# Kernel optimization log

Measured on AMD Instinct MI355X. Metric: run time of the kernel, lower is better.

## Reference

```python
import jax, jax.numpy as jnp
import numpy as np

B, DIM, HEADS, AGENT = 16, 256, 8, 49
POOL = 7  # int(sqrt(agent_num))


def _pool_matrix(size, out):
    # PyTorch AdaptiveAvgPool2d bin boundaries: start=floor(i*size/out), end=ceil((i+1)*size/out)
    P = np.zeros((out, size), np.float32)
    for i in range(out):
        s = (i * size) // out
        e = -((-(i + 1) * size) // out)
        P[i, s:e] = 1.0 / (e - s)
    return jnp.asarray(P)


def _forward(x, Wq, Wkv, Wproj, bproj, Wdwc, bdwc,
             an_bias, na_bias, ah_bias, aw_bias, ha_bias, wa_bias, H, W):
    b, c, h, w = x.shape
    n = H * W
    head_dim = c // HEADS
    scale = head_dim ** -0.5
    xt = x.reshape(b, c, n).transpose(0, 2, 1)            # [b, n, c]
    q = xt @ Wq.T                                          # [b, n, c]
    kv = xt @ Wkv.T
    k, v = jnp.split(kv, 2, axis=-1)
    # agent tokens: adaptive avg pool of q over the HxW grid -> 7x7
    qimg = q.reshape(b, H, W, c)
    Ph, Pw = _pool_matrix(H, POOL), _pool_matrix(W, POOL)
    agent = jnp.einsum('ph,qw,bhwc->bpqc', Ph, Pw, qimg).reshape(b, AGENT, c)

    def to_heads(t):
        return t.reshape(b, -1, HEADS, head_dim).transpose(0, 2, 1, 3)

    qh, kh, vh, ah = to_heads(q), to_heads(k), to_heads(v), to_heads(agent)

    # stage 1: agent -> kv attention with interpolated position bias
    pb1 = jax.image.resize(an_bias, (HEADS, AGENT, H, W), method='bilinear').reshape(HEADS, AGENT, n)
    pb2 = (ah_bias + aw_bias).reshape(1, HEADS, AGENT, n)
    pos_bias = pb1[None] + pb2                             # [1/b, h, 49, n]
    agent_attn = jax.nn.softmax(jnp.einsum('bhad,bhnd->bhan', ah * scale, kh) + pos_bias, axis=-1)
    agent_v = jnp.einsum('bhan,bhnd->bhad', agent_attn, vh)  # [b, h, 49, d]

    # stage 2: query -> agent attention
    ab1 = jax.image.resize(na_bias, (HEADS, AGENT, H, W), method='bilinear').reshape(HEADS, AGENT, n).transpose(0, 2, 1)
    ab2 = (ha_bias + wa_bias).reshape(1, HEADS, n, AGENT)
    agent_bias = ab1[None] + ab2                           # [1/b, h, n, 49]
    q_attn = jax.nn.softmax(jnp.einsum('bhnd,bhad->bhna', qh * scale, ah) + agent_bias, axis=-1)
    out = jnp.einsum('bhna,bhad->bhnd', q_attn, agent_v).transpose(0, 2, 1, 3).reshape(b, n, c)

    # depthwise conv residual on v
    vimg = vh.transpose(0, 2, 1, 3).reshape(b, H, W, c).transpose(0, 3, 1, 2)  # [b, c, H, W]
    dw = jax.lax.conv_general_dilated(vimg, Wdwc, (1, 1), 'SAME',
                                      feature_group_count=c,
                                      dimension_numbers=('NCHW', 'OIHW', 'NCHW'))
    dw = dw + bdwc[None, :, None, None]
    out = out + dw.transpose(0, 2, 3, 1).reshape(b, n, c)
    out = out @ Wproj.T + bproj
    return out.transpose(0, 2, 1).reshape(b, c, h, w)


def setup_inputs() -> dict:
    key = jax.random.key(0)
    ks = jax.random.split(key, 12)
    s = 0.02
    return {
        'x': jax.random.normal(ks[0], (B, DIM, 64, 64), jnp.float32),
        'Wq': jax.random.normal(ks[1], (DIM, DIM), jnp.float32) * s,
        'Wkv': jax.random.normal(ks[2], (2 * DIM, DIM), jnp.float32) * s,
        'Wproj': jax.random.normal(ks[3], (DIM, DIM), jnp.float32) * s,
        'bproj': jnp.zeros((DIM,), jnp.float32),
        'Wdwc': jax.random.normal(ks[4], (DIM, 1, 3, 3), jnp.float32) * s,
        'bdwc': jnp.zeros((DIM,), jnp.float32),
        'an_bias': jax.random.normal(ks[5], (HEADS, AGENT, 7, 7), jnp.float32) * s,
        'na_bias': jax.random.normal(ks[6], (HEADS, AGENT, 7, 7), jnp.float32) * s,
        'ah_bias': jax.random.normal(ks[7], (1, HEADS, AGENT, 64, 1), jnp.float32) * s,
        'aw_bias': jax.random.normal(ks[8], (1, HEADS, AGENT, 1, 64), jnp.float32) * s,
        'ha_bias': jax.random.normal(ks[9], (1, HEADS, 64, 1, AGENT), jnp.float32) * s,
        'wa_bias': jax.random.normal(ks[10], (1, HEADS, 1, 64, AGENT), jnp.float32) * s,
        'H': 64,
        'W': 64,
    }


def reference(x, Wq, Wkv, Wproj, bproj, Wdwc, bdwc,
              an_bias, na_bias, ah_bias, aw_bias, ha_bias, wa_bias, H, W):
    return _forward(x, Wq, Wkv, Wproj, bproj, Wdwc, bdwc,
                    an_bias, na_bias, ah_bias, aw_bias, ha_bias, wa_bias, H, W)
```

## Files before the change

### kernel.cpp

```cpp
#include <hip/hip_runtime.h>
#include <hip/hip_bf16.h>
#include <stdint.h>

using bf16 = __hip_bfloat16;

#define SCALE 0.17677669529663687f

typedef short short8 __attribute__((ext_vector_type(8)));
typedef float f32x4 __attribute__((ext_vector_type(4)));

__device__ __forceinline__ float bf2f(bf16 v) { return __bfloat162float(v); }

__device__ __forceinline__ unsigned short f2bf(float f) {
    unsigned int u = __float_as_uint(f);
    unsigned int r = u + 0x7fffu + ((u >> 16) & 1u);
    return (unsigned short)(r >> 16);
}

__device__ __forceinline__ void load8bf(const bf16* p, float* f) {
    uint4 u = *reinterpret_cast<const uint4*>(p);
    f[0] = __uint_as_float(u.x << 16); f[1] = __uint_as_float(u.x & 0xffff0000u);
    f[2] = __uint_as_float(u.y << 16); f[3] = __uint_as_float(u.y & 0xffff0000u);
    f[4] = __uint_as_float(u.z << 16); f[5] = __uint_as_float(u.z & 0xffff0000u);
    f[6] = __uint_as_float(u.w << 16); f[7] = __uint_as_float(u.w & 0xffff0000u);
}

__device__ __forceinline__ void gload16(const void* g, void* l) {
    __builtin_amdgcn_global_load_lds(
        (const __attribute__((address_space(1))) void*)g,
        (__attribute__((address_space(3))) void*)l, 16, 0, 0);
}

__global__ __launch_bounds__(256) void convert_w(
    const float* __restrict__ Wq, const float* __restrict__ Wkv,
    const float* __restrict__ Wp,
    bf16* __restrict__ Wqkv_bf, bf16* __restrict__ Wp_bf)
{
    int row = blockIdx.x, tid = threadIdx.x;
    const float* src; bf16* dst;
    if (row < 768) {
        src = (row < 256) ? Wq + (size_t)row * 256 : Wkv + (size_t)(row - 256) * 256;
        dst = Wqkv_bf + (size_t)row * 256;
    } else {
        src = Wp + (size_t)(row - 768) * 256;
        dst = Wp_bf + (size_t)(row - 768) * 256;
    }
    *reinterpret_cast<unsigned short*>(dst + tid) = f2bf(src[tid]);
}

__global__ __launch_bounds__(256) void x_to_bf16T(
    const float* __restrict__ x, bf16* __restrict__ xT)
{
    __shared__ float t[64][65];
    const int b = blockIdx.z, pos0 = blockIdx.x * 64, c0 = blockIdx.y * 64;
    const int tid = threadIdx.x;
    const int cc = tid >> 6, p = tid & 63;
    #pragma unroll
    for (int i = 0; i < 16; ++i)
        t[cc + 4 * i][p] = x[((size_t)(b * 256 + c0 + cc + 4 * i)) * 4096 + pos0 + p];
    __syncthreads();
    const int pl = tid >> 2, qd = tid & 3;
    unsigned short tmp[16];
    #pragma unroll
    for (int j = 0; j < 16; ++j) tmp[j] = f2bf(t[qd * 16 + j][pl]);
    uint4* dst = reinterpret_cast<uint4*>(xT + ((size_t)(b * 4096 + pos0 + pl)) * 256 + c0 + qd * 16);
    dst[0] = reinterpret_cast<const uint4*>(tmp)[0];
    dst[1] = reinterpret_cast<const uint4*>(tmp)[1];
}

__global__ __launch_bounds__(256) void qkv_mfma(
    const bf16* __restrict__ xT, const bf16* __restrict__ Wqkv,
    bf16* __restrict__ q, bf16* __restrict__ k, bf16* __restrict__ v)
{
    __shared__ __align__(16) short As[128 * 32];
    __shared__ __align__(16) short Bs[128 * 32];
    const int b = blockIdx.x >> 5;
    const int m0 = (blockIdx.x & 31) * 128;
    const int j0 = blockIdx.y * 128;
    const int tid = threadIdx.x;
    const int w = tid >> 6, lane = tid & 63;
    const int wm = w & 1, wn = w >> 1;
    const int quad = lane >> 4, ln = lane & 15;

    const short* Ag = (const short*)xT + ((size_t)(b * 4096 + m0)) * 256;
    const short* Bg = (const short*)Wqkv + (size_t)j0 * 256;
    const int ldrow = lane >> 2;
    const int ldcol = (lane & 3) * 8;

    f32x4 acc[4][4] = {};

    for (int k0 = 0; k0 < 256; k0 += 32) {
        __syncthreads();
        #pragma unroll
        for (int p = 0; p < 2; ++p) {
            int row = w * 32 + p * 16;
            gload16(Ag + (size_t)(row + ldrow) * 256 + k0 + ldcol, As + row * 32);
            gload16(Bg + (size_t)(row + ldrow) * 256 + k0 + ldcol, Bs + row * 32);
        }
        __syncthreads();
        short8 af[4], bfr[4];
        #pragma unroll
        for (int mi = 0; mi < 4; ++mi)
            af[mi] = *reinterpret_cast<const short8*>(&As[(wm * 64 + mi * 16 + ln) * 32 + quad * 8]);
        #pragma unroll
        for (int ni = 0; ni < 4; ++ni)
            bfr[ni] = *reinterpret_cast<const short8*>(&Bs[(wn * 64 + ni * 16 + ln) * 32 + quad * 8]);
        #pragma unroll
        for (int mi = 0; mi < 4; ++mi)
            #pragma unroll
            for (int ni = 0; ni < 4; ++ni)
                acc[mi][ni] = __builtin_amdgcn_mfma_f32_16x16x32_bf16(
                    af[mi], bfr[ni], acc[mi][ni], 0, 0, 0);
    }

    bf16* dst; int cb;
    if (j0 < 256)      { dst = q; cb = j0; }
    else if (j0 < 512) { dst = k; cb = j0 - 256; }
    else               { dst = v; cb = j0 - 512; }
    #pragma unroll
    for (int mi = 0; mi < 4; ++mi)
        #pragma unroll
        for (int r = 0; r < 4; ++r) {
            int pos = m0 + wm * 64 + mi * 16 + quad * 4 + r;
            unsigned short* o = reinterpret_cast<unsigned short*>(
                dst + ((size_t)(b * 4096 + pos)) * 256 + cb + wn * 64 + ln);
            #pragma unroll
            for (int ni = 0; ni < 4; ++ni)
                o[ni * 16] = f2bf(acc[mi][ni][r]);
        }
}

__global__ __launch_bounds__(256) void pool_agent(
    const bf16* __restrict__ q, float* __restrict__ agent)
{
    int bid = blockIdx.x;
    int b = bid / 49, a = bid % 49;
    int py = a / 7, px = a % 7;
    int ys = (py * 64) / 7, ye = ((py + 1) * 64 + 6) / 7;
    int xs = (px * 64) / 7, xe = ((px + 1) * 64 + 6) / 7;
    int ch = threadIdx.x;
    float s = 0.f;
    for (int y = ys; y < ye; ++y)
        for (int x = xs; x < xe; ++x)
            s += bf2f(q[((size_t)(b * 4096) + y * 64 + x) * 256 + ch]);
    agent[((size_t)(b * 49) + a) * 256 + ch] = s / (float)((ye - ys) * (xe - xs));
}

__global__ __launch_bounds__(256) void make_pbias(
    const float* __restrict__ an, const float* __restrict__ ahb,
    const float* __restrict__ awb, float* __restrict__ pbias)
{
    int bid = blockIdx.x;
    __shared__ float bb[49], ay[64], ax[64];
    int tid = threadIdx.x;
    if (tid < 49) bb[tid] = an[(size_t)bid * 49 + tid];
    if (tid < 64) {
        ay[tid] = ahb[(size_t)bid * 64 + tid];
        ax[tid] = awb[(size_t)bid * 64 + tid];
    }
    __syncthreads();
    for (int it = 0; it < 16; ++it) {
        int pos = it * 256 + tid;
        int y = pos >> 6, x = pos & 63;
        float fy = (y + 0.5f) * (7.f / 64.f) - 0.5f; fy = fminf(fmaxf(fy, 0.f), 6.f);
        float fx = (x + 0.5f) * (7.f / 64.f) - 0.5f; fx = fminf(fmaxf(fx, 0.f), 6.f);
        int y0 = (int)fy, x0 = (int)fx;
        int y1 = min(y0 + 1, 6), x1 = min(x0 + 1, 6);
        float wy = fy - y0, wx = fx - x0;
        float val = (1.f - wy) * ((1.f - wx) * bb[y0 * 7 + x0] + wx * bb[y0 * 7 + x1])
                  + wy * ((1.f - wx) * bb[y1 * 7 + x0] + wx * bb[y1 * 7 + x1]);
        pbias[(size_t)bid * 4096 + pos] = val + ay[y] + ax[x];
    }
}

__global__ __launch_bounds__(256) void make_abias2(
    const float* __restrict__ na, const float* __restrict__ hab,
    const float* __restrict__ wab, bf16* __restrict__ ab2)
{
    const int h = blockIdx.x, p0 = blockIdx.y * 256;
    const int tid = threadIdx.x;
    __shared__ float bb[49 * 49];
    __shared__ float hy[64 * 49];
    __shared__ float wxs[64 * 49];
    for (int i = tid; i < 49 * 49; i += 256) bb[i] = na[(size_t)h * 2401 + i];
    for (int i = tid; i < 64 * 49; i += 256) {
        hy[i]  = hab[(size_t)h * 3136 + i];
        wxs[i] = wab[(size_t)h * 3136 + i];
    }
    __syncthreads();
    const int pos = p0 + tid;
    const int y = pos >> 6, x = pos & 63;
    float fy = (y + 0.5f) * (7.f / 64.f) - 0.5f; fy = fminf(fmaxf(fy, 0.f), 6.f);
    float fx = (x + 0.5f) * (7.f / 64.f) - 0.5f; fx = fminf(fmaxf(fx, 0.f), 6.f);
    int y0 = (int)fy, x0 = (int)fx;
    int y1 = min(y0 + 1, 6), x1 = min(x0 + 1, 6);
    float wy = fy - y0, wxv = fx - x0;
    float w00 = (1.f - wy) * (1.f - wxv), w01 = (1.f - wy) * wxv;
    float w10 = wy * (1.f - wxv),        w11 = wy * wxv;
    int g00 = y0 * 7 + x0, g01 = y0 * 7 + x1, g10 = y1 * 7 + x0, g11 = y1 * 7 + x1;
    unsigned short outv[64];
    #pragma unroll
    for (int a = 0; a < 64; ++a) {
        float val = 0.f;
        if (a < 49)
            val = w00 * bb[a * 49 + g00] + w01 * bb[a * 49 + g01]
                + w10 * bb[a * 49 + g10] + w11 * bb[a * 49 + g11]
                + hy[y * 49 + a] + wxs[x * 49 + a];
        outv[(a & 15) * 4 + (a >> 4)] = f2bf(val);
    }
    uint4* dst = reinterpret_cast<uint4*>(
        reinterpret_cast<unsigned short*>(ab2) + ((size_t)(h * 4096) + pos) * 64);
    #pragma unroll
    for (int j = 0; j < 8; ++j) dst[j] = reinterpret_cast<const uint4*>(outv)[j];
}

__global__ __launch_bounds__(256) void stage1(
    const float* __restrict__ agent, const bf16* __restrict__ k,
    const bf16* __restrict__ v, const float* __restrict__ pbias,
    float* __restrict__ part_O, float* __restrict__ part_sum)
{
    const int bid = blockIdx.x;
    const int split = bid & 7, h = (bid >> 3) & 7, b = bid >> 6;
    const int tid = threadIdx.x;
    const int w = tid >> 6, lane = tid & 63;
    const int ln = lane & 15, quad = lane >> 4;

    __shared__ __align__(16) short agLds[64 * 32];
    __shared__ __align__(16) short pLds[64 * 140];
    __shared__ __align__(16) short vtLds[32 * 140];

    for (int i = tid; i < 64 * 32; i += 256) {
        int a = i >> 5, d = i & 31;
        float val = (a < 49) ? agent[((size_t)(b * 49) + a) * 256 + h * 32 + d] : 0.f;
        agLds[i] = (short)f2bf(val);
    }
    __syncthreads();

    const short8 agFrag = *reinterpret_cast<const short8*>(&agLds[(w * 16 + ln) * 32 + quad * 8]);
    const int a_row = w * 16 + quad * 4;

    f32x4 oAcc[2] = {};
    float sacc[4] = {0.f, 0.f, 0.f, 0.f};
    const f32x4 zero4 = {0.f, 0.f, 0.f, 0.f};

    for (int sub = 0; sub < 4; ++sub) {
        const int nbase = split * 512 + sub * 128;
        __syncthreads();
        {
            const int n_loc = tid & 127, dh = (tid >> 7) * 16;
            const short* vr = (const short*)v + ((size_t)(b * 4096) + nbase + n_loc) * 256 + h * 32 + dh;
            uint4 u0 = *reinterpret_cast<const uint4*>(vr);
            uint4 u1 = *reinterpret_cast<const uint4*>(vr + 8);
            unsigned int uu[8] = {u0.x, u0.y, u0.z, u0.w, u1.x, u1.y, u1.z, u1.w};
            #pragma unroll
            for (int j = 0; j < 8; ++j) {
                vtLds[(dh + 2 * j) * 140 + n_loc]     = (short)(uu[j] & 0xffffu);
                vtLds[(dh + 2 * j + 1) * 140 + n_loc] = (short)(uu[j] >> 16);
            }
        }
        short8 kf[8];
        #pragma unroll
        for (int t = 0; t < 8; ++t) {
            int n = nbase + t * 16 + ln;
            kf[t] = *reinterpret_cast<const short8*>(
                (const short*)k + ((size_t)(b * 4096) + n) * 256 + h * 32 + quad * 8);
        }
        #pragma unroll
        for (int t = 0; t < 8; ++t) {
            f32x4 s = __builtin_amdgcn_mfma_f32_16x16x32_bf16(agFrag, kf[t], zero4, 0, 0, 0);
            int n = nbase + t * 16 + ln;
            #pragma unroll
            for (int r = 0; r < 4; ++r) {
                int a = a_row + r;
                float e = 0.f;
                if (a < 49) {
                    float sv = s[r] * SCALE + pbias[((size_t)(h * 49) + a) * 4096 + n];
                    e = __expf(sv);
                }
                sacc[r] += e;
                pLds[(a_row + r) * 140 + t * 16 + ln] = (short)f2bf(e);
            }
        }
        __syncthreads();
        #pragma unroll
        for (int ks = 0; ks < 4; ++ks) {
            short8 pf = *reinterpret_cast<const short8*>(&pLds[(w * 16 + ln) * 140 + ks * 32 + quad * 8]);
            #pragma unroll
            for (int dt = 0; dt < 2; ++dt) {
                short8 vf = *reinterpret_cast<const short8*>(&vtLds[(dt * 16 + ln) * 140 + ks * 32 + quad * 8]);
                oAcc[dt] = __builtin_amdgcn_mfma_f32_16x16x32_bf16(pf, vf, oAcc[dt], 0, 0, 0);
            }
        }
    }

    const size_t obase = ((size_t)((b * 8 + h) * 8 + split)) * 1568;
    #pragma unroll
    for (int dt = 0; dt < 2; ++dt)
        #pragma unroll
        for (int r = 0; r < 4; ++r) {
            int a = a_row + r;
            if (a < 49)
                part_O[obase + a * 32 + dt * 16 + ln] = oAcc[dt][r];
        }
    #pragma unroll
    for (int r = 0; r < 4; ++r) {
        float sv = sacc[r];
        #pragma unroll
        for (int m = 1; m < 16; m <<= 1) sv += __shfl_xor(sv, m, 64);
        if (ln == 0) {
            int a = a_row + r;
            if (a < 49)
                part_sum[((b * 8 + h) * 8 + split) * 49 + a] = sv;
        }
    }
}

__global__ __launch_bounds__(256) void stage1_fin(
    const float* __restrict__ part_O, const float* __restrict__ part_sum,
    bf16* __restrict__ avT)
{
    int bh = blockIdx.x;
    __shared__ float inv[49];
    int tid = threadIdx.x;
    if (tid < 49) {
        float s = 0.f;
        #pragma unroll
        for (int sp = 0; sp < 8; ++sp) s += part_sum[(bh * 8 + sp) * 49 + tid];
        inv[tid] = 1.f / s;
    }
    __syncthreads();
    unsigned short* dst = reinterpret_cast<unsigned short*>(avT) + (size_t)bh * 2048;
    for (int i = tid; i < 2048; i += 256) {
        int d = i >> 6, a = i & 63;
        float val = 0.f;
        if (a < 49) {
            float o = 0.f;
            #pragma unroll
            for (int sp = 0; sp < 8; ++sp)
                o += part_O[((size_t)(bh * 8) + sp) * 1568 + a * 32 + d];
            val = o * inv[a];
        }
        dst[i] = f2bf(val);
    }
}

__global__ __launch_bounds__(256) void stage2_mfma(
    const bf16* __restrict__ q, const bf16* __restrict__ v,
    const float* __restrict__ agent, const bf16* __restrict__ avT,
    const bf16* __restrict__ ab2, const float* __restrict__ wdwc,
    const float* __restrict__ bdwc, bf16* __restrict__ mid)
{
    const int bh = blockIdx.x;
    const int b = bh >> 3, h = bh & 7;
    const int base = blockIdx.y * 256;
    const int tid = threadIdx.x;
    const int w = tid >> 6, lane = tid & 63;
    const int quad = lane >> 4, ln = lane & 15;

    __shared__ __align__(16) short agLds[64 * 32];
    __shared__ __align__(16) short pLds[4][16 * 72];
    __shared__ __align__(16) float oLds[2][64 * 36];
    __shared__ float wdLds[32 * 9];
    __shared__ float bdLds[32];

    for (int i = tid; i < 64 * 32; i += 256) {
        int a = i >> 5, d = i & 31;
        float val = (a < 49) ? agent[((size_t)(b * 49) + a) * 256 + h * 32 + d] : 0.f;
        agLds[i] = (short)f2bf(val);
    }
    for (int i = tid; i < 288; i += 256) wdLds[i] = wdwc[(size_t)(h * 32) * 9 + i];
    if (tid < 32) bdLds[tid] = bdwc[h * 32 + tid];
    __syncthreads();

    short8 agF[4];
    #pragma unroll
    for (int t = 0; t < 4; ++t)
        agF[t] = *reinterpret_cast<const short8*>(&agLds[(t * 16 + ln) * 32 + quad * 8]);

    short8 avF[2][2];
    #pragma unroll
    for (int dt = 0; dt < 2; ++dt)
        #pragma unroll
        for (int kc = 0; kc < 2; ++kc)
            avF[dt][kc] = *reinterpret_cast<const short8*>(
                (const short*)avT + ((size_t)bh * 32 + dt * 16 + ln) * 64 + kc * 32 + quad * 8);

    const int prow = tid >> 2, cl = (tid & 3) * 8;
    const f32x4 zero4 = {0.f, 0.f, 0.f, 0.f};

    for (int sub = 0; sub < 4; ++sub) {
        const int p = sub & 1;
        const int pos0w = base + sub * 64 + w * 16;

        const int posd = base + sub * 64 + prow;
        const int yd = posd >> 6, xd = posd & 63;
        uint4 vpre[9];
        #pragma unroll
        for (int dy = -1; dy <= 1; ++dy)
            #pragma unroll
            for (int dx = -1; dx <= 1; ++dx) {
                int idx = (dy + 1) * 3 + (dx + 1);
                int yy = yd + dy, xx = xd + dx;
                int yc = min(max(yy, 0), 63), xc = min(max(xx, 0), 63);
                uint4 t = *reinterpret_cast<const uint4*>(
                    v + ((size_t)(b * 4096) + yc * 64 + xc) * 256 + h * 32 + cl);
                if ((unsigned)yy >= 64u || (unsigned)xx >= 64u) { t.x = 0; t.y = 0; t.z = 0; t.w = 0; }
                vpre[idx] = t;
            }

        uint2 bpre[4];
        #pragma unroll
        for (int r = 0; r < 4; ++r) {
            int posr = pos0w + quad * 4 + r;
            bpre[r] = *reinterpret_cast<const uint2*>(
                reinterpret_cast<const unsigned short*>(ab2) + ((size_t)(h * 4096) + posr) * 64 + ln * 4);
        }

        short8 qf = *reinterpret_cast<const short8*>(
            (const short*)q + ((size_t)(b * 4096) + pos0w + ln) * 256 + h * 32 + quad * 8);
        f32x4 sT[4];
        #pragma unroll
        for (int t = 0; t < 4; ++t)
            sT[t] = __builtin_amdgcn_mfma_f32_16x16x32_bf16(qf, agF[t], zero4, 0, 0, 0);

        float e[4][4];
        float part[4] = {0.f, 0.f, 0.f, 0.f};
        #pragma unroll
        for (int r = 0; r < 4; ++r) {
            float bias[4];
            bias[0] = __uint_as_float(bpre[r].x << 16);
            bias[1] = __uint_as_float(bpre[r].x & 0xffff0000u);
            bias[2] = __uint_as_float(bpre[r].y << 16);
            bias[3] = __uint_as_float(bpre[r].y & 0xffff0000u);
            #pragma unroll
            for (int t = 0; t < 4; ++t) {
                int a = t * 16 + ln;
                float ev = 0.f;
                if (a < 49) ev = __expf(sT[t][r] * SCALE + bias[t]);
                e[t][r] = ev;
                part[r] += ev;
            }
        }
        #pragma unroll
        for (int r = 0; r < 4; ++r) {
            #pragma unroll
            for (int m = 1; m < 16; m <<= 1) part[r] += __shfl_xor(part[r], m, 64);
            part[r] = 1.f / part[r];
        }

        #pragma unroll
        for (int t = 0; t < 4; ++t)
            #pragma unroll
            for (int r = 0; r < 4; ++r)
                pLds[w][(quad * 4 + r) * 72 + t * 16 + ln] = (short)f2bf(e[t][r] * part[r]);

        f32x4 oAcc[2] = {};
        #pragma unroll
        for (int kc = 0; kc < 2; ++kc) {
            short8 pf = *reinterpret_cast<const short8*>(&pLds[w][ln * 72 + kc * 32 + quad * 8]);
            #pragma unroll
            for (int dt = 0; dt < 2; ++dt)
                oAcc[dt] = __builtin_amdgcn_mfma_f32_16x16x32_bf16(pf, avF[dt][kc], oAcc[dt], 0, 0, 0);
        }

        #pragma unroll
        for (int dt = 0; dt < 2; ++dt)
            #pragma unroll
            for (int r = 0; r < 4; ++r)
                oLds[p][(w * 16 + quad * 4 + r) * 36 + dt * 16 + ln] = oAcc[dt][r];
        __syncthreads();

        {
            float acc[8];
            #pragma unroll
            for (int j = 0; j < 8; ++j) acc[j] = oLds[p][prow * 36 + cl + j] + bdLds[cl + j];
            #pragma unroll
            for (int idx = 0; idx < 9; ++idx) {
                unsigned int uu[4] = {vpre[idx].x, vpre[idx].y, vpre[idx].z, vpre[idx].w};
                float f[8];
                f[0] = __uint_as_float(uu[0] << 16); f[1] = __uint_as_float(uu[0] & 0xffff0000u);
                f[2] = __uint_as_float(uu[1] << 16); f[3] = __uint_as_float(uu[1] & 0xffff0000u);
                f[4] = __uint_as_float(uu[2] << 16); f[5] = __uint_as_float(uu[2] & 0xffff0000u);
                f[6] = __uint_as_float(uu[3] << 16); f[7] = __uint_as_float(uu[3] & 0xffff0000u);
                #pragma unroll
                for (int j = 0; j < 8; ++j)
                    acc[j] = fmaf(wdLds[(cl + j) * 9 + idx], f[j], acc[j]);
            }
            unsigned short o16[8];
            #pragma unroll
            for (int j = 0; j < 8; ++j) o16[j] = f2bf(acc[j]);
            *reinterpret_cast<uint4*>(mid + ((size_t)(b * 4096) + posd) * 256 + h * 32 + cl) =
                *reinterpret_cast<const uint4*>(o16);
        }
    }
}

__global__ __launch_bounds__(256) void proj_mfma(
    const bf16* __restrict__ mid, const bf16* __restrict__ Wp,
    const float* __restrict__ bp, float* __restrict__ out)
{
    __shared__ __align__(16) short As[128 * 32];
    __shared__ __align__(16) short Bs[128 * 32];
    const int m0 = blockIdx.x * 128;
    const int b  = blockIdx.y >> 5;
    const int n0 = (blockIdx.y & 31) * 128;
    const int tid = threadIdx.x;
    const int w = tid >> 6, lane = tid & 63;
    const int wm = w & 1, wn = w >> 1;
    const int quad = lane >> 4, ln = lane & 15;

    const short* Ag = (const short*)Wp + (size_t)m0 * 256;
    const short* Bg = (const short*)mid + ((size_t)(b * 4096 + n0)) * 256;
    const int ldrow = lane >> 2;
    const int ldcol = (lane & 3) * 8;

    f32x4 acc[4][4] = {};

    for (int k0 = 0; k0 < 256; k0 += 32) {
        __syncthreads();
        #pragma unroll
        for (int p = 0; p < 2; ++p) {
            int row = w * 32 + p * 16;
            gload16(Ag + (size_t)(row + ldrow) * 256 + k0 + ldcol, As + row * 32);
            gload16(Bg + (size_t)(row + ldrow) * 256 + k0 + ldcol, Bs + row * 32);
        }
        __syncthreads();
        short8 af[4], bfr[4];
        #pragma unroll
        for (int mi = 0; mi < 4; ++mi)
            af[mi] = *reinterpret_cast<const short8*>(&As[(wm * 64 + mi * 16 + ln) * 32 + quad * 8]);
        #pragma unroll
        for (int ni = 0; ni < 4; ++ni)
            bfr[ni] = *reinterpret_cast<const short8*>(&Bs[(wn * 64 + ni * 16 + ln) * 32 + quad * 8]);
        #pragma unroll
        for (int mi = 0; mi < 4; ++mi)
            #pragma unroll
            for (int ni = 0; ni < 4; ++ni)
                acc[mi][ni] = __builtin_amdgcn_mfma_f32_16x16x32_bf16(
                    af[mi], bfr[ni], acc[mi][ni], 0, 0, 0);
    }

    #pragma unroll
    for (int mi = 0; mi < 4; ++mi)
        #pragma unroll
        for (int r = 0; r < 4; ++r) {
            int ch = m0 + wm * 64 + mi * 16 + quad * 4 + r;
            float bias = bp[ch];
            float* o = out + ((size_t)(b * 256 + ch)) * 4096 + n0 + wn * 64 + ln;
            #pragma unroll
            for (int ni = 0; ni < 4; ++ni)
                o[ni * 16] = acc[mi][ni][r] + bias;
        }
}

extern "C" void kernel_launch(void* const* d_in, const int* in_sizes, int n_in,
                              void* d_out, int out_size, void* d_ws, size_t ws_size,
                              hipStream_t stream)
{
    const float* x       = (const float*)d_in[0];
    const float* Wq      = (const float*)d_in[1];
    const float* Wkv     = (const float*)d_in[2];
    const float* Wproj   = (const float*)d_in[3];
    const float* bproj   = (const float*)d_in[4];
    const float* Wdwc    = (const float*)d_in[5];
    const float* bdwc    = (const float*)d_in[6];
    const float* an_bias = (const float*)d_in[7];
    const float* na_bias = (const float*)d_in[8];
    const float* ah_bias = (const float*)d_in[9];
    const float* aw_bias = (const float*)d_in[10];
    const float* ha_bias = (const float*)d_in[11];
    const float* wa_bias = (const float*)d_in[12];

    char* ws = (char*)d_ws;
    bf16*  q      = (bf16*)(ws + 0);
    bf16*  k      = (bf16*)(ws + 33554432);
    bf16*  v      = (bf16*)(ws + 67108864);
    bf16*  xT     = (bf16*)(ws + 100663296);
    float* part_O   = (float*)(ws + 100663296);
    float* part_sum = (float*)(ws + 100663296 + 6422528);
    bf16*  mid    = (bf16*)(ws + 100663296);
    float* agent  = (float*)(ws + 134217728);
    bf16*  avT    = (bf16*)(ws + 135020544);
    float* pbias  = (float*)(ws + 135823360);
    bf16*  ab2    = (bf16*)(ws + 142245888);
    bf16*  Wqkv_bf = (bf16*)(ws + 148668416);
    bf16*  Wp_bf   = (bf16*)(ws + 149061632);
    float* out    = (float*)d_out;

    convert_w  <<<dim3(1024),      256, 0, stream>>>(Wq, Wkv, Wproj, Wqkv_bf, Wp_bf);
    x_to_bf16T <<<dim3(64, 4, 16), 256, 0, stream>>>(x, xT);
    qkv_mfma   <<<dim3(512, 6),    256, 0, stream>>>(xT, Wqkv_bf, q, k, v);
    pool_agent <<<dim3(784),       256, 0, stream>>>(q, agent);
    make_pbias <<<dim3(392),       256, 0, stream>>>(an_bias, ah_bias, aw_bias, pbias);
    make_abias2<<<dim3(8, 16),     256, 0, stream>>>(na_bias, ha_bias, wa_bias, ab2);
    stage1     <<<dim3(1024),      256, 0, stream>>>(agent, k, v, pbias, part_O, part_sum);
    stage1_fin <<<dim3(128),       256, 0, stream>>>(part_O, part_sum, avT);
    stage2_mfma<<<dim3(128, 16),   256, 0, stream>>>(q, v, agent, avT, ab2, Wdwc, bdwc, mid);
    proj_mfma  <<<dim3(2, 512),    256, 0, stream>>>(mid, Wp_bf, bproj, out);
}
```

Before: 371.8 us.

## Fuse fp32-to-bf16 transpose of x into the QKV GEMM A-tile load

Removes the separate x_to_bf16T kernel and its bf16 xT intermediate. The QKV GEMM now reads x directly in fp32 channel-major layout, converts it to bf16 and transposes it into a padded shared-memory A tile. The grid is reordered so the six output-column blocks sharing one x tile run next to each other, which should help L2 reuse of x. The cost is that each x tile is re-read and re-converted six times instead of once.

```diff
diff --git a/kernel.cpp b/kernel.cpp
--- a/kernel.cpp
+++ b/kernel.cpp
@@ -48,44 +48,26 @@
     *reinterpret_cast<unsigned short*>(dst + tid) = f2bf(src[tid]);
 }
 
-__global__ __launch_bounds__(256) void x_to_bf16T(
-    const float* __restrict__ x, bf16* __restrict__ xT)
-{
-    __shared__ float t[64][65];
-    const int b = blockIdx.z, pos0 = blockIdx.x * 64, c0 = blockIdx.y * 64;
-    const int tid = threadIdx.x;
-    const int cc = tid >> 6, p = tid & 63;
-    #pragma unroll
-    for (int i = 0; i < 16; ++i)
-        t[cc + 4 * i][p] = x[((size_t)(b * 256 + c0 + cc + 4 * i)) * 4096 + pos0 + p];
-    __syncthreads();
-    const int pl = tid >> 2, qd = tid & 3;
-    unsigned short tmp[16];
-    #pragma unroll
-    for (int j = 0; j < 16; ++j) tmp[j] = f2bf(t[qd * 16 + j][pl]);
-    uint4* dst = reinterpret_cast<uint4*>(xT + ((size_t)(b * 4096 + pos0 + pl)) * 256 + c0 + qd * 16);
-    dst[0] = reinterpret_cast<const uint4*>(tmp)[0];
-    dst[1] = reinterpret_cast<const uint4*>(tmp)[1];
-}
-
 __global__ __launch_bounds__(256) void qkv_mfma(
-    const bf16* __restrict__ xT, const bf16* __restrict__ Wqkv,
+    const float* __restrict__ x, const bf16* __restrict__ Wqkv,
     bf16* __restrict__ q, bf16* __restrict__ k, bf16* __restrict__ v)
 {
-    __shared__ __align__(16) short As[128 * 32];
+    __shared__ __align__(16) short As[128 * 36];
     __shared__ __align__(16) short Bs[128 * 32];
-    const int b = blockIdx.x >> 5;
-    const int m0 = (blockIdx.x & 31) * 128;
-    const int j0 = blockIdx.y * 128;
+    const int j0 = blockIdx.x * 128;
+    const int b  = blockIdx.y >> 5;
+    const int m0 = (blockIdx.y & 31) * 128;
     const int tid = threadIdx.x;
     const int w = tid >> 6, lane = tid & 63;
     const int wm = w & 1, wn = w >> 1;
     const int quad = lane >> 4, ln = lane & 15;
 
-    const short* Ag = (const short*)xT + ((size_t)(b * 4096 + m0)) * 256;
+    const float* Ax = x + (size_t)(b * 256) * 4096 + m0;
     const short* Bg = (const short*)Wqkv + (size_t)j0 * 256;
     const int ldrow = lane >> 2;
     const int ldcol = (lane & 3) * 8;
+    const int c4 = (tid >> 5) * 4;
+    const int p4 = (tid & 31) * 4;
 
     f32x4 acc[4][4] = {};
 
@@ -94,14 +76,28 @@
         #pragma unroll
         for (int p = 0; p < 2; ++p) {
             int row = w * 32 + p * 16;
-            gload16(Ag + (size_t)(row + ldrow) * 256 + k0 + ldcol, As + row * 32);
             gload16(Bg + (size_t)(row + ldrow) * 256 + k0 + ldcol, Bs + row * 32);
         }
+        float4 xr[4];
+        #pragma unroll
+        for (int j = 0; j < 4; ++j)
+            xr[j] = *reinterpret_cast<const float4*>(
+                Ax + (size_t)(k0 + c4 + j) * 4096 + p4);
+        #pragma unroll
+        for (int pp = 0; pp < 4; ++pp) {
+            unsigned short t4[4];
+            t4[0] = f2bf(((const float*)&xr[0])[pp]);
+            t4[1] = f2bf(((const float*)&xr[1])[pp]);
+            t4[2] = f2bf(((const float*)&xr[2])[pp]);
+            t4[3] = f2bf(((const float*)&xr[3])[pp]);
+            *reinterpret_cast<uint2*>(&As[(p4 + pp) * 36 + c4]) =
+                *reinterpret_cast<const uint2*>(t4);
+        }
         __syncthreads();
         short8 af[4], bfr[4];
         #pragma unroll
         for (int mi = 0; mi < 4; ++mi)
-            af[mi] = *reinterpret_cast<const short8*>(&As[(wm * 64 + mi * 16 + ln) * 32 + quad * 8]);
+            af[mi] = *reinterpret_cast<const short8*>(&As[(wm * 64 + mi * 16 + ln) * 36 + quad * 8]);
         #pragma unroll
         for (int ni = 0; ni < 4; ++ni)
             bfr[ni] = *reinterpret_cast<const short8*>(&Bs[(wn * 64 + ni * 16 + ln) * 32 + quad * 8]);
@@ -575,7 +571,6 @@
     bf16*  q      = (bf16*)(ws + 0);
     bf16*  k      = (bf16*)(ws + 33554432);
     bf16*  v      = (bf16*)(ws + 67108864);
-    bf16*  xT     = (bf16*)(ws + 100663296);
     float* part_O   = (float*)(ws + 100663296);
     float* part_sum = (float*)(ws + 100663296 + 6422528);
     bf16*  mid    = (bf16*)(ws + 100663296);
@@ -588,8 +583,7 @@
     float* out    = (float*)d_out;
 
     convert_w  <<<dim3(1024),      256, 0, stream>>>(Wq, Wkv, Wproj, Wqkv_bf, Wp_bf);
-    x_to_bf16T <<<dim3(64, 4, 16), 256, 0, stream>>>(x, xT);
-    qkv_mfma   <<<dim3(512, 6),    256, 0, stream>>>(xT, Wqkv_bf, q, k, v);
+    qkv_mfma   <<<dim3(6, 512),    256, 0, stream>>>(x, Wqkv_bf, q, k, v);
     pool_agent <<<dim3(784),       256, 0, stream>>>(q, agent);
     make_pbias <<<dim3(392),       256, 0, stream>>>(an_bias, ah_bias, aw_bias, pbias);
     make_abias2<<<dim3(8, 16),     256, 0, stream>>>(na_bias, ha_bias, wa_bias, ab2);
```

Result: no change. 376.9 us (+1.4%).
